# Performance work log

Measured on AMD Instinct MI355X. Metric: run time of the kernel, lower is better.

The kernel has to match this reference:

```python
import jax, jax.numpy as jnp
import numpy as np

H = 1024   # hidden_size
B = 4096   # batch
C = 2      # num_classes

def setup_inputs() -> dict:
    key = jax.random.key(0)
    ks = jax.random.split(key, 12)
    s = 0.02
    return {
        "h": jax.random.normal(ks[0], (2, B, H), jnp.float32),
        "c": jax.random.normal(ks[1], (2, B, H), jnp.float32),
        # torch nn.LSTM params: W_ih_l0 (4H, C), W_hh_l0 (4H, H), biases (4H,)
        "W_ih0": jax.random.normal(ks[2], (4 * H, C), jnp.float32) * s,
        "W_hh0": jax.random.normal(ks[3], (4 * H, H), jnp.float32) * s,
        "b_ih0": jax.random.normal(ks[4], (4 * H,), jnp.float32) * s,
        "b_hh0": jax.random.normal(ks[5], (4 * H,), jnp.float32) * s,
        "W_ih1": jax.random.normal(ks[6], (4 * H, H), jnp.float32) * s,
        "W_hh1": jax.random.normal(ks[7], (4 * H, H), jnp.float32) * s,
        "b_ih1": jax.random.normal(ks[8], (4 * H,), jnp.float32) * s,
        "b_hh1": jax.random.normal(ks[9], (4 * H,), jnp.float32) * s,
        "fc_W": jax.random.normal(ks[10], (C, H), jnp.float32) * s,
        "fc_b": jax.random.normal(ks[11], (C,), jnp.float32) * s,
        "pred_len": 64,
    }

def _lstm_cell(gates, c_prev):
    # torch gate order: input, forget, cell(g), output
    i, f, g, o = jnp.split(gates, 4, axis=1)
    c_new = jax.nn.sigmoid(f) * c_prev + jax.nn.sigmoid(i) * jnp.tanh(g)
    h_new = jax.nn.sigmoid(o) * jnp.tanh(c_new)
    return h_new, c_new

def reference(h, c, W_ih0, W_hh0, b_ih0, b_hh0, W_ih1, W_hh1, b_ih1, b_hh1, fc_W, fc_b, pred_len):
    h0, h1 = h[0], h[1]
    c0, c1 = c[0], c[1]
    x0 = jnp.zeros((h0.shape[0], fc_W.shape[0]), h.dtype)  # (B, C)

    def step(carry, _):
        h0, c0, h1, c1, x = carry
        g0 = x @ W_ih0.T + b_ih0 + h0 @ W_hh0.T + b_hh0
        h0n, c0n = _lstm_cell(g0, c0)
        g1 = h0n @ W_ih1.T + b_ih1 + h1 @ W_hh1.T + b_hh1
        h1n, c1n = _lstm_cell(g1, c1)
        logit = h1n @ fc_W.T + fc_b                       # (B, C)
        # greedy argmax feedback (targets=None branch)
        x_next = jax.nn.one_hot(jnp.argmax(logit, axis=1), logit.shape[1], dtype=logit.dtype)
        return (h0n, c0n, h1n, c1n, x_next), logit

    _, logits = jax.lax.scan(step, (h0, c0, h1, c1, x0), None, length=pred_len)
    return jnp.transpose(logits, (1, 0, 2))  # (B, pred_len, C)
```

## Files before the change

kernel.cpp:

```cpp
#include <hip/hip_runtime.h>
#include <stdint.h>

#define H_ 1024
#define NG_ 4096

typedef float f32x4 __attribute__((ext_vector_type(4)));
typedef __bf16 bf16x8 __attribute__((ext_vector_type(8)));

__device__ __forceinline__ unsigned short f2bf(float f) {
  union { float f; uint32_t u; } v; v.f = f;
  uint32_t r = v.u + 0x7FFFu + ((v.u >> 16) & 1u);
  return (unsigned short)(r >> 16);
}
__device__ __forceinline__ float bf2f(unsigned short b) {
  union { uint32_t u; float f; } v; v.u = ((uint32_t)b) << 16; return v.f;
}

__device__ __forceinline__ void gload_lds16(const void* g, void* l) {
  __builtin_amdgcn_global_load_lds(
      (const __attribute__((address_space(1))) void*)g,
      (__attribute__((address_space(3))) void*)l, 16, 0, 0);
}

__device__ __forceinline__ float sigm(float x) { return 1.f / (1.f + __expf(-x)); }
__device__ __forceinline__ float tanh_(float x) { return 1.f - 2.f / (__expf(2.f * x) + 1.f); }

__global__ void prep_w0(const float* __restrict__ Whh0, unsigned short* __restrict__ Wr) {
  int i = (blockIdx.x * 256 + threadIdx.x) * 4;
  int r = i >> 10, k = i & 1023;
  int gate = (r >> 4) & 3;
  int j = ((r >> 6) << 4) + (r & 15);
  const float4 v = *(const float4*)(Whh0 + (size_t)(gate * H_ + j) * H_ + k);
  ushort4 o; o.x = f2bf(v.x); o.y = f2bf(v.y); o.z = f2bf(v.z); o.w = f2bf(v.w);
  *(ushort4*)(Wr + i) = o;
}

__global__ void prep_wcat(const float* __restrict__ Wih1, const float* __restrict__ Whh1,
                          unsigned short* __restrict__ Wr) {
  int i = (blockIdx.x * 256 + threadIdx.x) * 4;
  int r = i >> 11, k = i & 2047;
  int gate = (r >> 4) & 3;
  int j = ((r >> 6) << 4) + (r & 15);
  const float* src = (k < 1024) ? (Wih1 + (size_t)(gate * H_ + j) * H_ + k)
                                : (Whh1 + (size_t)(gate * H_ + j) * H_ + (k - 1024));
  const float4 v = *(const float4*)src;
  ushort4 o; o.x = f2bf(v.x); o.y = f2bf(v.y); o.z = f2bf(v.z); o.w = f2bf(v.w);
  *(ushort4*)(Wr + (size_t)r * 2048 + k) = o;
}

__global__ void prep_small(const float* __restrict__ Wih0,
                           const float* __restrict__ bih0, const float* __restrict__ bhh0,
                           const float* __restrict__ bih1, const float* __restrict__ bhh1,
                           float* __restrict__ bias0r, float* __restrict__ bias1r,
                           float* __restrict__ wi0r) {
  int r = blockIdx.x * 256 + threadIdx.x;
  int gate = (r >> 4) & 3;
  int j = ((r >> 6) << 4) + (r & 15);
  int old = gate * H_ + j;
  bias0r[r] = bih0[old] + bhh0[old];
  bias1r[r] = bih1[old] + bhh1[old];
  wi0r[r * 2 + 0] = Wih0[old * 2 + 0];
  wi0r[r * 2 + 1] = Wih0[old * 2 + 1];
}

__global__ void prep_state(const float* __restrict__ h, const float* __restrict__ c,
                           unsigned short* __restrict__ h0b, unsigned short* __restrict__ h1b,
                           float* __restrict__ c0, float* __restrict__ c1, int bh) {
  int i = (blockIdx.x * 256 + threadIdx.x) * 4;
  float4 a = *(const float4*)(h + i);
  float4 b = *(const float4*)(h + (size_t)bh + i);
  ushort4 oa; oa.x = f2bf(a.x); oa.y = f2bf(a.y); oa.z = f2bf(a.z); oa.w = f2bf(a.w);
  ushort4 ob; ob.x = f2bf(b.x); ob.y = f2bf(b.y); ob.z = f2bf(b.z); ob.w = f2bf(b.w);
  *(ushort4*)(h0b + i) = oa;
  *(ushort4*)(h1b + i) = ob;
  *(float4*)(c0 + i) = *(const float4*)(c + i);
  *(float4*)(c1 + i) = *(const float4*)(c + (size_t)bh + i);
}

__global__ void lstm_gemm_cell(const unsigned short* __restrict__ A0,
                               const unsigned short* __restrict__ A1,
                               int Ktot,
                               const unsigned short* __restrict__ Bw,
                               const float* __restrict__ biasr,
                               const float* __restrict__ wi0r,
                               const int* __restrict__ xidx,
                               int have_x,
                               float* __restrict__ Cst,
                               unsigned short* __restrict__ Hout) {
  __shared__ unsigned short As[128 * 64];
  __shared__ unsigned short Bs[128 * 64];
  const int tid  = threadIdx.x;
  const int lane = tid & 63;
  const int wv   = tid >> 6;
  const int wm   = wv >> 1, wn = wv & 1;
  const int tile_m = blockIdx.y * 128;
  const int tile_n = blockIdx.x * 128;

  f32x4 acc[4][4];
#pragma unroll
  for (int m = 0; m < 4; ++m)
#pragma unroll
    for (int n = 0; n < 4; ++n) acc[m][n] = (f32x4)0.f;

  const int lrow = lane >> 3;
  const int lk   = ((lane & 7) ^ lrow) * 8;

  const int nk = Ktot >> 6;
  for (int kt = 0; kt < nk; ++kt) {
    const int k0 = kt << 6;
    const unsigned short* Ap; int kl;
    if (k0 < 1024) { Ap = A0; kl = k0; } else { Ap = A1; kl = k0 - 1024; }
#pragma unroll
    for (int i = 0; i < 4; ++i) {
      int chunk = wv * 4 + i;
      int row = chunk * 8 + lrow;
      gload_lds16(Ap + (size_t)(tile_m + row) * H_ + kl + lk, (void*)&As[chunk * 512]);
    }
#pragma unroll
    for (int i = 0; i < 4; ++i) {
      int chunk = wv * 4 + i;
      int row = chunk * 8 + lrow;
      gload_lds16(Bw + (size_t)(tile_n + row) * Ktot + k0 + lk, (void*)&Bs[chunk * 512]);
    }
    __syncthreads();

    const char* Ab = (const char*)As;
    const char* Bb = (const char*)Bs;
    const int arow = wm * 64 + (lane & 15);
    const int brow = wn * 64 + (lane & 15);
    const int khi  = lane >> 4;
    const int x7   = lane & 7;
    const int ksw0 = ((0 + khi) ^ x7) * 16;
    const int ksw1 = ((4 + khi) ^ x7) * 16;
#pragma unroll
    for (int ks = 0; ks < 2; ++ks) {
      const int ksw = ks ? ksw1 : ksw0;
      bf16x8 af[4], bfr[4];
#pragma unroll
      for (int m = 0; m < 4; ++m)
        af[m] = *(const bf16x8*)(Ab + (arow + m * 16) * 128 + ksw);
#pragma unroll
      for (int n = 0; n < 4; ++n)
        bfr[n] = *(const bf16x8*)(Bb + (brow + n * 16) * 128 + ksw);
#pragma unroll
      for (int m = 0; m < 4; ++m)
#pragma unroll
        for (int n = 0; n < 4; ++n)
          acc[m][n] = __builtin_amdgcn_mfma_f32_16x16x32_bf16(af[m], bfr[n], acc[m][n], 0, 0, 0);
    }
    __syncthreads();
  }

  const int cl = lane & 15;
  const int rq = (lane >> 4) * 4;
  const int jgrp = (tile_n >> 6) + wn;
  const int j = jgrp * 16 + cl;
  float bias[4], w0v[4] = {0, 0, 0, 0}, w1v[4] = {0, 0, 0, 0};
#pragma unroll
  for (int n = 0; n < 4; ++n) {
    int colr = tile_n + wn * 64 + n * 16 + cl;
    bias[n] = biasr[colr];
    if (have_x) { w0v[n] = wi0r[colr * 2]; w1v[n] = wi0r[colr * 2 + 1]; }
  }
#pragma unroll
  for (int m = 0; m < 4; ++m) {
#pragma unroll
    for (int q = 0; q < 4; ++q) {
      int row = tile_m + wm * 64 + m * 16 + rq + q;
      float gi = acc[m][0][q] + bias[0];
      float gf = acc[m][1][q] + bias[1];
      float gg = acc[m][2][q] + bias[2];
      float go = acc[m][3][q] + bias[3];
      if (have_x) {
        int x = xidx[row];
        gi += x ? w1v[0] : w0v[0];
        gf += x ? w1v[1] : w0v[1];
        gg += x ? w1v[2] : w0v[2];
        go += x ? w1v[3] : w0v[3];
      }
      size_t off = (size_t)row * H_ + j;
      float cp = Cst[off];
      float cn = sigm(gf) * cp + sigm(gi) * tanh_(gg);
      float hn = sigm(go) * tanh_(cn);
      Cst[off] = cn;
      Hout[off] = f2bf(hn);
    }
  }
}

__global__ void fc_argmax(const unsigned short* __restrict__ h1,
                          const float* __restrict__ fcW, const float* __restrict__ fcb,
                          float* __restrict__ out, int* __restrict__ xidx,
                          int t, int pred_len) {
  const int lane = threadIdx.x & 63;
  const int wv = threadIdx.x >> 6;
  const int row = blockIdx.x * 4 + wv;
  const unsigned short* hp = h1 + (size_t)row * H_ + lane * 16;
  float d0 = 0.f, d1 = 0.f;
#pragma unroll
  for (int u = 0; u < 2; ++u) {
    ushort4 ha = *(const ushort4*)(hp + u * 8);
    ushort4 hb = *(const ushort4*)(hp + u * 8 + 4);
    float hv[8] = { bf2f(ha.x), bf2f(ha.y), bf2f(ha.z), bf2f(ha.w),
                    bf2f(hb.x), bf2f(hb.y), bf2f(hb.z), bf2f(hb.w) };
#pragma unroll
    for (int e = 0; e < 8; ++e) {
      int k = lane * 16 + u * 8 + e;
      d0 += hv[e] * fcW[k];
      d1 += hv[e] * fcW[H_ + k];
    }
  }
#pragma unroll
  for (int off = 32; off > 0; off >>= 1) {
    d0 += __shfl_xor(d0, off);
    d1 += __shfl_xor(d1, off);
  }
  if (lane == 0) {
    d0 += fcb[0]; d1 += fcb[1];
    size_t o = ((size_t)row * pred_len + t) * 2;
    out[o] = d0; out[o + 1] = d1;
    xidx[row] = (d1 > d0) ? 1 : 0;
  }
}

extern "C" void kernel_launch(void* const* d_in, const int* in_sizes, int n_in,
                              void* d_out, int out_size, void* d_ws, size_t ws_size,
                              hipStream_t stream) {
  const float* h     = (const float*)d_in[0];
  const float* c     = (const float*)d_in[1];
  const float* Wih0  = (const float*)d_in[2];
  const float* Whh0  = (const float*)d_in[3];
  const float* bih0  = (const float*)d_in[4];
  const float* bhh0  = (const float*)d_in[5];
  const float* Wih1  = (const float*)d_in[6];
  const float* Whh1  = (const float*)d_in[7];
  const float* bih1  = (const float*)d_in[8];
  const float* bhh1  = (const float*)d_in[9];
  const float* fcW   = (const float*)d_in[10];
  const float* fcb   = (const float*)d_in[11];

  const int B = in_sizes[0] / (2 * H_);
  const int pred_len = out_size / (B * 2);
  const int BH = B * H_;

  size_t off = 0;
  auto carve = [&](size_t bytes) -> void* {
    void* p = (char*)d_ws + off;
    off += (bytes + 255) & ~(size_t)255;
    return p;
  };
  unsigned short* Whh0r = (unsigned short*)carve((size_t)NG_ * 1024 * 2);
  unsigned short* Wcatr = (unsigned short*)carve((size_t)NG_ * 2048 * 2);
  unsigned short* h0b[2], *h1b[2];
  h0b[0] = (unsigned short*)carve((size_t)BH * 2);
  h0b[1] = (unsigned short*)carve((size_t)BH * 2);
  h1b[0] = (unsigned short*)carve((size_t)BH * 2);
  h1b[1] = (unsigned short*)carve((size_t)BH * 2);
  float* c0 = (float*)carve((size_t)BH * 4);
  float* c1 = (float*)carve((size_t)BH * 4);
  float* bias0r = (float*)carve(NG_ * 4);
  float* bias1r = (float*)carve(NG_ * 4);
  float* wi0r   = (float*)carve(NG_ * 2 * 4);
  int*   xidx   = (int*)carve(B * 4);

  hipLaunchKernelGGL(prep_w0,   dim3((NG_ * 1024 / 4) / 256), dim3(256), 0, stream, Whh0, Whh0r);
  hipLaunchKernelGGL(prep_wcat, dim3((NG_ * 2048 / 4) / 256), dim3(256), 0, stream, Wih1, Whh1, Wcatr);
  hipLaunchKernelGGL(prep_small, dim3(NG_ / 256), dim3(256), 0, stream,
                     Wih0, bih0, bhh0, bih1, bhh1, bias0r, bias1r, wi0r);
  hipLaunchKernelGGL(prep_state, dim3((BH / 4) / 256), dim3(256), 0, stream,
                     h, c, h0b[0], h1b[0], c0, c1, BH);

  dim3 ggrid(NG_ / 128, B / 128);
  dim3 gblk(256);
  float* out = (float*)d_out;

  for (int t = 0; t < pred_len; ++t) {
    const int cur = t & 1, nxt = cur ^ 1;
    hipLaunchKernelGGL(lstm_gemm_cell, ggrid, gblk, 0, stream,
                       h0b[cur], (const unsigned short*)nullptr, 1024, Whh0r,
                       bias0r, wi0r, xidx, (t > 0) ? 1 : 0, c0, h0b[nxt]);
    hipLaunchKernelGGL(lstm_gemm_cell, ggrid, gblk, 0, stream,
                       h0b[nxt], h1b[cur], 2048, Wcatr,
                       bias1r, (const float*)nullptr, (const int*)nullptr, 0, c1, h1b[nxt]);
    hipLaunchKernelGGL(fc_argmax, dim3(B / 4), dim3(256), 0, stream,
                       h1b[nxt], fcW, fcb, out, xidx, t, pred_len);
  }
}
```

Measured before the change: 7.339 ms.

## Fuse FC projection and argmax feedback into layer-1 GEMM epilogue with atomics

Removes the separate fc_argmax kernel. The layer-1 GEMM epilogue now computes partial FC dot products from fp32 h, reduces them across 16 lanes with shuffles and accumulates them into the zero-initialised output with atomicAdd. The next step's layer-0 kernel reads the previous logits straight from the output to pick the one-hot input. It also adds launch bounds and a workgroup-id swizzle to improve L2 reuse. The trade is one fewer launch and h1 reread per step against many float atomics, and the summation order is no longer deterministic.

```diff
diff --git a/kernel.cpp b/kernel.cpp
--- a/kernel.cpp
+++ b/kernel.cpp
@@ -77,24 +77,31 @@
   *(float4*)(c1 + i) = *(const float4*)(c + (size_t)bh + i);
 }
 
-__global__ void lstm_gemm_cell(const unsigned short* __restrict__ A0,
-                               const unsigned short* __restrict__ A1,
-                               int Ktot,
-                               const unsigned short* __restrict__ Bw,
-                               const float* __restrict__ biasr,
-                               const float* __restrict__ wi0r,
-                               const int* __restrict__ xidx,
-                               int have_x,
-                               float* __restrict__ Cst,
-                               unsigned short* __restrict__ Hout) {
+__global__ void __launch_bounds__(256, 4)
+lstm_gemm_cell(const unsigned short* __restrict__ A0,
+               const unsigned short* __restrict__ A1,
+               int Ktot,
+               const unsigned short* __restrict__ Bw,
+               const float* __restrict__ biasr,
+               const float* __restrict__ wi0r,
+               const float* __restrict__ xlog,
+               float* __restrict__ Cst,
+               unsigned short* __restrict__ Hout,
+               const float* __restrict__ fcW,
+               const float* __restrict__ fcb,
+               float* __restrict__ outT,
+               int pl2) {
   __shared__ unsigned short As[128 * 64];
   __shared__ unsigned short Bs[128 * 64];
   const int tid  = threadIdx.x;
   const int lane = tid & 63;
   const int wv   = tid >> 6;
   const int wm   = wv >> 1, wn = wv & 1;
-  const int tile_m = blockIdx.y * 128;
-  const int tile_n = blockIdx.x * 128;
+
+  const int wgid = blockIdx.y * 32 + blockIdx.x;
+  const int swz  = ((wgid & 7) << 7) | (wgid >> 3);
+  const int tile_m = (swz >> 5) * 128;
+  const int tile_n = (swz & 31) * 128;
 
   f32x4 acc[4][4];
 #pragma unroll
@@ -156,12 +163,17 @@
   const int jgrp = (tile_n >> 6) + wn;
   const int j = jgrp * 16 + cl;
   float bias[4], w0v[4] = {0, 0, 0, 0}, w1v[4] = {0, 0, 0, 0};
+  const int have_x = (xlog != nullptr);
 #pragma unroll
   for (int n = 0; n < 4; ++n) {
     int colr = tile_n + wn * 64 + n * 16 + cl;
     bias[n] = biasr[colr];
     if (have_x) { w0v[n] = wi0r[colr * 2]; w1v[n] = wi0r[colr * 2 + 1]; }
   }
+  float fW0 = 0.f, fW1 = 0.f;
+  if (fcW) { fW0 = fcW[j]; fW1 = fcW[H_ + j]; }
+  const int add_bias = (tile_n == 0) && (wn == 0);
+
 #pragma unroll
   for (int m = 0; m < 4; ++m) {
 #pragma unroll
@@ -172,7 +184,8 @@
       float gg = acc[m][2][q] + bias[2];
       float go = acc[m][3][q] + bias[3];
       if (have_x) {
-        int x = xidx[row];
+        const float* xr = xlog + (size_t)row * pl2;
+        int x = xr[1] > xr[0];
         gi += x ? w1v[0] : w0v[0];
         gf += x ? w1v[1] : w0v[1];
         gg += x ? w1v[2] : w0v[2];
@@ -184,42 +197,21 @@
       float hn = sigm(go) * tanh_(cn);
       Cst[off] = cn;
       Hout[off] = f2bf(hn);
-    }
-  }
-}
-
-__global__ void fc_argmax(const unsigned short* __restrict__ h1,
-                          const float* __restrict__ fcW, const float* __restrict__ fcb,
-                          float* __restrict__ out, int* __restrict__ xidx,
-                          int t, int pred_len) {
-  const int lane = threadIdx.x & 63;
-  const int wv = threadIdx.x >> 6;
-  const int row = blockIdx.x * 4 + wv;
-  const unsigned short* hp = h1 + (size_t)row * H_ + lane * 16;
-  float d0 = 0.f, d1 = 0.f;
-#pragma unroll
-  for (int u = 0; u < 2; ++u) {
-    ushort4 ha = *(const ushort4*)(hp + u * 8);
-    ushort4 hb = *(const ushort4*)(hp + u * 8 + 4);
-    float hv[8] = { bf2f(ha.x), bf2f(ha.y), bf2f(ha.z), bf2f(ha.w),
-                    bf2f(hb.x), bf2f(hb.y), bf2f(hb.z), bf2f(hb.w) };
-#pragma unroll
-    for (int e = 0; e < 8; ++e) {
-      int k = lane * 16 + u * 8 + e;
-      d0 += hv[e] * fcW[k];
-      d1 += hv[e] * fcW[H_ + k];
-    }
-  }
-#pragma unroll
-  for (int off = 32; off > 0; off >>= 1) {
-    d0 += __shfl_xor(d0, off);
-    d1 += __shfl_xor(d1, off);
-  }
-  if (lane == 0) {
-    d0 += fcb[0]; d1 += fcb[1];
-    size_t o = ((size_t)row * pred_len + t) * 2;
-    out[o] = d0; out[o + 1] = d1;
-    xidx[row] = (d1 > d0) ? 1 : 0;
+      if (fcW) {
+        float d0 = hn * fW0, d1 = hn * fW1;
+#pragma unroll
+        for (int s = 1; s < 16; s <<= 1) {
+          d0 += __shfl_xor(d0, s);
+          d1 += __shfl_xor(d1, s);
+        }
+        if (cl == 0) {
+          if (add_bias) { d0 += fcb[0]; d1 += fcb[1]; }
+          float* op = outT + (size_t)row * pl2;
+          atomicAdd(op, d0);
+          atomicAdd(op + 1, d1);
+        }
+      }
+    }
   }
 }
 
@@ -242,6 +234,7 @@
   const int B = in_sizes[0] / (2 * H_);
   const int pred_len = out_size / (B * 2);
   const int BH = B * H_;
+  const int pl2 = pred_len * 2;
 
   size_t off = 0;
   auto carve = [&](size_t bytes) -> void* {
@@ -261,7 +254,8 @@
   float* bias0r = (float*)carve(NG_ * 4);
   float* bias1r = (float*)carve(NG_ * 4);
   float* wi0r   = (float*)carve(NG_ * 2 * 4);
-  int*   xidx   = (int*)carve(B * 4);
+
+  hipMemsetAsync(d_out, 0, (size_t)out_size * sizeof(float), stream);
 
   hipLaunchKernelGGL(prep_w0,   dim3((NG_ * 1024 / 4) / 256), dim3(256), 0, stream, Whh0, Whh0r);
   hipLaunchKernelGGL(prep_wcat, dim3((NG_ * 2048 / 4) / 256), dim3(256), 0, stream, Wih1, Whh1, Wcatr);
@@ -278,11 +272,15 @@
     const int cur = t & 1, nxt = cur ^ 1;
     hipLaunchKernelGGL(lstm_gemm_cell, ggrid, gblk, 0, stream,
                        h0b[cur], (const unsigned short*)nullptr, 1024, Whh0r,
-                       bias0r, wi0r, xidx, (t > 0) ? 1 : 0, c0, h0b[nxt]);
+                       bias0r, wi0r,
+                       (t > 0) ? (out + (size_t)(t - 1) * 2) : (const float*)nullptr,
+                       c0, h0b[nxt],
+                       (const float*)nullptr, (const float*)nullptr, (float*)nullptr, pl2);
     hipLaunchKernelGGL(lstm_gemm_cell, ggrid, gblk, 0, stream,
                        h0b[nxt], h1b[cur], 2048, Wcatr,
-                       bias1r, (const float*)nullptr, (const int*)nullptr, 0, c1, h1b[nxt]);
-    hipLaunchKernelGGL(fc_argmax, dim3(B / 4), dim3(256), 0, stream,
-                       h1b[nxt], fcW, fcb, out, xidx, t, pred_len);
-  }
-}
+                       bias1r, (const float*)nullptr,
+                       (const float*)nullptr,
+                       c1, h1b[nxt],
+                       fcW, fcb, out + (size_t)t * 2, pl2);
+  }
+}
```

Result: slower. 8.648 ms (+17.8%).

## Hoist layer-1 recurrent GEMM into layer-0 launch with bf16 partial-gate buffer

Applied to the files above, without the earlier changes.

Computes the h1·W_hh1 contribution of layer 1 in extra blocks of the layer-0 kernel, since it does not depend on the new h0, and stores the partial gates as bf16 in a workspace. The layer-1 kernel then runs only the K=1024 h0·W_ih1 part and adds the stored partials before the cell update. This balances the two launches and increases parallelism in the first one, at the cost of extra global traffic for the partial buffer and bf16 rounding of the partial sums. It also adds launch bounds for occupancy.

```diff
diff --git a/kernel.cpp b/kernel.cpp
--- a/kernel.cpp
+++ b/kernel.cpp
@@ -77,24 +77,34 @@
   *(float4*)(c1 + i) = *(const float4*)(c + (size_t)bh + i);
 }
 
-__global__ void lstm_gemm_cell(const unsigned short* __restrict__ A0,
-                               const unsigned short* __restrict__ A1,
-                               int Ktot,
-                               const unsigned short* __restrict__ Bw,
-                               const float* __restrict__ biasr,
-                               const float* __restrict__ wi0r,
-                               const int* __restrict__ xidx,
-                               int have_x,
-                               float* __restrict__ Cst,
-                               unsigned short* __restrict__ Hout) {
+__global__ void __launch_bounds__(256, 4)
+lstm_step(const unsigned short* __restrict__ A,
+          const unsigned short* __restrict__ Bw, int KsB,
+          const float* __restrict__ biasr,
+          const float* __restrict__ wi0r,
+          const int* __restrict__ xidx, int have_x,
+          float* __restrict__ Cst,
+          unsigned short* __restrict__ Hout,
+          const unsigned short* __restrict__ Gin,
+          int myb,
+          const unsigned short* __restrict__ A2,
+          const unsigned short* __restrict__ Bw2, int KsB2,
+          unsigned short* __restrict__ Gout) {
   __shared__ unsigned short As[128 * 64];
   __shared__ unsigned short Bs[128 * 64];
   const int tid  = threadIdx.x;
   const int lane = tid & 63;
   const int wv   = tid >> 6;
   const int wm   = wv >> 1, wn = wv & 1;
-  const int tile_m = blockIdx.y * 128;
-  const int tile_n = blockIdx.x * 128;
+
+  const int by = blockIdx.y, bx = blockIdx.x;
+  const bool gmode = (A2 != nullptr) && (by >= myb);
+  const unsigned short* Ap = gmode ? A2 : A;
+  const unsigned short* Bp = gmode ? Bw2 : Bw;
+  const int Ks  = gmode ? KsB2 : KsB;
+  const int tmb = gmode ? (by - myb) : by;
+  const int tile_m = tmb * 128;
+  const int tile_n = bx * 128;
 
   f32x4 acc[4][4];
 #pragma unroll
@@ -105,22 +115,19 @@
   const int lrow = lane >> 3;
   const int lk   = ((lane & 7) ^ lrow) * 8;
 
-  const int nk = Ktot >> 6;
-  for (int kt = 0; kt < nk; ++kt) {
+  for (int kt = 0; kt < 16; ++kt) {
     const int k0 = kt << 6;
-    const unsigned short* Ap; int kl;
-    if (k0 < 1024) { Ap = A0; kl = k0; } else { Ap = A1; kl = k0 - 1024; }
 #pragma unroll
     for (int i = 0; i < 4; ++i) {
       int chunk = wv * 4 + i;
       int row = chunk * 8 + lrow;
-      gload_lds16(Ap + (size_t)(tile_m + row) * H_ + kl + lk, (void*)&As[chunk * 512]);
+      gload_lds16(Ap + (size_t)(tile_m + row) * H_ + k0 + lk, (void*)&As[chunk * 512]);
     }
 #pragma unroll
     for (int i = 0; i < 4; ++i) {
       int chunk = wv * 4 + i;
       int row = chunk * 8 + lrow;
-      gload_lds16(Bw + (size_t)(tile_n + row) * Ktot + k0 + lk, (void*)&Bs[chunk * 512]);
+      gload_lds16(Bp + (size_t)(tile_n + row) * Ks + k0 + lk, (void*)&Bs[chunk * 512]);
     }
     __syncthreads();
 
@@ -149,6 +156,35 @@
           acc[m][n] = __builtin_amdgcn_mfma_f32_16x16x32_bf16(af[m], bfr[n], acc[m][n], 0, 0, 0);
     }
     __syncthreads();
+  }
+
+  if (gmode) {
+    uint32_t* gp = (uint32_t*)Gout + ((size_t)(tmb * gridDim.x + bx) << 13) + tid;
+#pragma unroll
+    for (int m = 0; m < 4; ++m)
+#pragma unroll
+      for (int n = 0; n < 4; ++n)
+#pragma unroll
+        for (int q2 = 0; q2 < 2; ++q2) {
+          uint32_t v = (uint32_t)f2bf(acc[m][n][q2 * 2]) |
+                       ((uint32_t)f2bf(acc[m][n][q2 * 2 + 1]) << 16);
+          gp[(m * 8 + n * 2 + q2) * 256] = v;
+        }
+    return;
+  }
+
+  if (Gin) {
+    const uint32_t* gp = (const uint32_t*)Gin + ((size_t)(by * gridDim.x + bx) << 13) + tid;
+#pragma unroll
+    for (int m = 0; m < 4; ++m)
+#pragma unroll
+      for (int n = 0; n < 4; ++n)
+#pragma unroll
+        for (int q2 = 0; q2 < 2; ++q2) {
+          uint32_t v = gp[(m * 8 + n * 2 + q2) * 256];
+          acc[m][n][q2 * 2]     += bf2f((unsigned short)(v & 0xffff));
+          acc[m][n][q2 * 2 + 1] += bf2f((unsigned short)(v >> 16));
+        }
   }
 
   const int cl = lane & 15;
@@ -242,6 +278,7 @@
   const int B = in_sizes[0] / (2 * H_);
   const int pred_len = out_size / (B * 2);
   const int BH = B * H_;
+  const int MB = B / 128;
 
   size_t off = 0;
   auto carve = [&](size_t bytes) -> void* {
@@ -262,6 +299,7 @@
   float* bias1r = (float*)carve(NG_ * 4);
   float* wi0r   = (float*)carve(NG_ * 2 * 4);
   int*   xidx   = (int*)carve(B * 4);
+  unsigned short* G1p = (unsigned short*)carve((size_t)B * NG_ * 2);
 
   hipLaunchKernelGGL(prep_w0,   dim3((NG_ * 1024 / 4) / 256), dim3(256), 0, stream, Whh0, Whh0r);
   hipLaunchKernelGGL(prep_wcat, dim3((NG_ * 2048 / 4) / 256), dim3(256), 0, stream, Wih1, Whh1, Wcatr);
@@ -270,18 +308,26 @@
   hipLaunchKernelGGL(prep_state, dim3((BH / 4) / 256), dim3(256), 0, stream,
                      h, c, h0b[0], h1b[0], c0, c1, BH);
 
-  dim3 ggrid(NG_ / 128, B / 128);
+  dim3 ggridA(NG_ / 128, MB * 2);
+  dim3 ggridB(NG_ / 128, MB);
   dim3 gblk(256);
   float* out = (float*)d_out;
 
   for (int t = 0; t < pred_len; ++t) {
     const int cur = t & 1, nxt = cur ^ 1;
-    hipLaunchKernelGGL(lstm_gemm_cell, ggrid, gblk, 0, stream,
-                       h0b[cur], (const unsigned short*)nullptr, 1024, Whh0r,
-                       bias0r, wi0r, xidx, (t > 0) ? 1 : 0, c0, h0b[nxt]);
-    hipLaunchKernelGGL(lstm_gemm_cell, ggrid, gblk, 0, stream,
-                       h0b[nxt], h1b[cur], 2048, Wcatr,
-                       bias1r, (const float*)nullptr, (const int*)nullptr, 0, c1, h1b[nxt]);
+    hipLaunchKernelGGL(lstm_step, ggridA, gblk, 0, stream,
+                       h0b[cur], Whh0r, 1024,
+                       bias0r, wi0r, xidx, (t > 0) ? 1 : 0,
+                       c0, h0b[nxt],
+                       (const unsigned short*)nullptr,
+                       MB, h1b[cur], Wcatr + 1024, 2048, G1p);
+    hipLaunchKernelGGL(lstm_step, ggridB, gblk, 0, stream,
+                       h0b[nxt], Wcatr, 2048,
+                       bias1r, (const float*)nullptr, (const int*)nullptr, 0,
+                       c1, h1b[nxt],
+                       G1p,
+                       MB, (const unsigned short*)nullptr,
+                       (const unsigned short*)nullptr, 0, (unsigned short*)nullptr);
     hipLaunchKernelGGL(fc_argmax, dim3(B / 4), dim3(256), 0, stream,
                        h1b[nxt], fcW, fcb, out, xidx, t, pred_len);
   }
```

Result: slower. 8.586 ms (+17.0%).
